# Kernel optimization log

Measured on AMD Instinct MI355X. Metric: run time of the kernel, lower is better.

Reference implementation:

```python
import jax, jax.numpy as jnp
import numpy as np
import math

H = 8
C = 512
HIDE = 2048
LN_EPS = 1e-6


def setup_inputs() -> dict:
    key = jax.random.key(0)
    ks = jax.random.split(key, 9)
    B, N = 4, 2048
    std = 0.02
    return {
        "q": jax.random.normal(ks[0], (B, N, C), jnp.float32),
        "k": jax.random.normal(ks[1], (B, N, C), jnp.float32),
        "v": jax.random.normal(ks[2], (B, N, C), jnp.float32),
        "fc1_w": jax.random.normal(ks[3], (HIDE, C), jnp.float32) * std,
        "fc1_b": jnp.zeros((HIDE,), jnp.float32),
        "fc2_w": jax.random.normal(ks[4], (C, HIDE), jnp.float32) * std,
        "fc2_b": jnp.zeros((C,), jnp.float32),
        "ln1_w": jnp.ones((C,), jnp.float32),
        "ln1_b": jnp.zeros((C,), jnp.float32),
        "ln2_w": jnp.ones((C,), jnp.float32),
        "ln2_b": jnp.zeros((C,), jnp.float32),
    }


def _layernorm(x, w, b):
    mu = jnp.mean(x, axis=-1, keepdims=True)
    var = jnp.var(x, axis=-1, keepdims=True)
    return (x - mu) * jax.lax.rsqrt(var + LN_EPS) * w + b


def _mha(q, k, v):
    B, N, _ = q.shape
    hd = C // H
    # [B, H, N, hd]
    qh = q.reshape(B, N, H, hd).transpose(0, 2, 1, 3)
    kh = k.reshape(B, N, H, hd).transpose(0, 2, 1, 3)
    vh = v.reshape(B, N, H, hd).transpose(0, 2, 1, 3)
    scores = jnp.einsum('bhqd,bhkd->bhqk', qh, kh) / math.sqrt(hd)
    probs = jax.nn.softmax(scores, axis=-1)
    out = jnp.einsum('bhqk,bhkd->bhqd', probs, vh)
    return out.transpose(0, 2, 1, 3).reshape(B, N, C)


def reference(q, k, v, fc1_w, fc1_b, fc2_w, fc2_b, ln1_w, ln1_b, ln2_w, ln2_b):
    attn = _mha(q, k, v)
    q2 = _layernorm(q + attn, ln1_w, ln1_b)
    h = jax.nn.gelu(q2 @ fc1_w.T + fc1_b, approximate=False)
    mlp = h @ fc2_w.T + fc2_b
    return _layernorm(q2 + mlp, ln2_w, ln2_b)
```

## Files before the change

kernel.cpp:

```cpp
#include <hip/hip_runtime.h>
#include <math.h>

typedef unsigned short u16;
typedef __bf16 bf16_t;
typedef bf16_t bf16x4 __attribute__((ext_vector_type(4)));
typedef bf16_t bf16x8 __attribute__((ext_vector_type(8)));
typedef short s16x4 __attribute__((ext_vector_type(4)));
typedef float f32x4 __attribute__((ext_vector_type(4)));

typedef const __attribute__((address_space(1))) void* gcp;
typedef __attribute__((address_space(3))) void* lcp;

#define BB 4
#define NN 2048
#define CC 512
#define HH 8
#define HD 64
#define HIDE_ 2048
#define TT (BB*NN)

#if __has_builtin(__builtin_amdgcn_exp2f)
#define EXP2(x) __builtin_amdgcn_exp2f(x)
#else
#define EXP2(x) __expf((x) * 0.69314718055994531f)
#endif

#if __has_builtin(__builtin_amdgcn_rcpf)
#define RCP(x) __builtin_amdgcn_rcpf(x)
#else
#define RCP(x) (1.0f / (x))
#endif

__device__ __forceinline__ u16 f2bf(float f) {
  unsigned u = __float_as_uint(f);
  u += 0x7FFF + ((u >> 16) & 1);
  return (u16)(u >> 16);
}

__device__ __forceinline__ int xcd_swz(int orig, int nwg) {
  return (orig & 7) * (nwg >> 3) + (orig >> 3);
}

__device__ __forceinline__ void bf8_to_f(const u16* p, float* f) {
  uint4 u = *(const uint4*)p;
  f[0] = __uint_as_float(u.x << 16); f[1] = __uint_as_float(u.x & 0xffff0000u);
  f[2] = __uint_as_float(u.y << 16); f[3] = __uint_as_float(u.y & 0xffff0000u);
  f[4] = __uint_as_float(u.z << 16); f[5] = __uint_as_float(u.z & 0xffff0000u);
  f[6] = __uint_as_float(u.w << 16); f[7] = __uint_as_float(u.w & 0xffff0000u);
}

__device__ __forceinline__ bf16x8 ldq8(const float* p, float s) {
  float4 a = *(const float4*)p;
  float4 b = *(const float4*)(p + 4);
  bf16x8 r = {(bf16_t)(a.x * s), (bf16_t)(a.y * s), (bf16_t)(a.z * s), (bf16_t)(a.w * s),
              (bf16_t)(b.x * s), (bf16_t)(b.y * s), (bf16_t)(b.z * s), (bf16_t)(b.w * s)};
  return r;
}

__device__ __forceinline__ float gelu_tanh(float x) {
  float y = 0.7978845608028654f * x * (1.0f + 0.044715f * x * x);
  float a = y * 2.8853900817779268f;
  a = fminf(fmaxf(a, -30.0f), 30.0f);
  float e = EXP2(a);
  float t = (e - 1.0f) * RCP(e + 1.0f);
  return 0.5f * x * (1.0f + t);
}

__global__ __launch_bounds__(256) void prep_kernel(const float* __restrict__ k,
                                                   const float* __restrict__ fc1w,
                                                   const float* __restrict__ fc2w,
                                                   const float* __restrict__ v,
                                                   u16* __restrict__ kb,
                                                   u16* __restrict__ w1b,
                                                   u16* __restrict__ w2b,
                                                   u16* __restrict__ vtb) {
  __shared__ __align__(16) u16 T[64 * 72];
  int bid = blockIdx.x, tid = threadIdx.x;
  if (bid < 3072) {
    const float* in;
    u16* out;
    int rel;
    if (bid < 2048)      { in = k;    out = kb;  rel = bid; }
    else if (bid < 2560) { in = fc1w; out = w1b; rel = bid - 2048; }
    else                 { in = fc2w; out = w2b; rel = bid - 2560; }
    int i = (rel * 256 + tid) * 8;
    float4 a = *(const float4*)(in + i);
    float4 b2 = *(const float4*)(in + i + 4);
    u16 r[8] = {f2bf(a.x), f2bf(a.y), f2bf(a.z), f2bf(a.w),
                f2bf(b2.x), f2bf(b2.y), f2bf(b2.z), f2bf(b2.w)};
    *(uint4*)(out + i) = *(const uint4*)r;
    return;
  }
  int tv = bid - 3072;
  int j0 = (tv & 31) * 64;
  int bh = tv >> 5;
  int b = bh >> 3, h = bh & 7;
#pragma unroll
  for (int i = 0; i < 4; i++) {
    int idx = i * 256 + tid;
    int j = idx >> 4, dq = idx & 15;
    float4 a = *(const float4*)(v + ((size_t)(b * NN + j0 + j)) * CC + h * 64 + dq * 4);
    T[(dq * 4 + 0) * 72 + j] = f2bf(a.x);
    T[(dq * 4 + 1) * 72 + j] = f2bf(a.y);
    T[(dq * 4 + 2) * 72 + j] = f2bf(a.z);
    T[(dq * 4 + 3) * 72 + j] = f2bf(a.w);
  }
  __syncthreads();
#pragma unroll
  for (int i = 0; i < 2; i++) {
    int idx = i * 256 + tid;
    int d = idx >> 3, jb = idx & 7;
    uint4 val = *(const uint4*)&T[d * 72 + jb * 8];
    *(uint4*)&vtb[((size_t)(bh * 64 + d)) * NN + j0 + jb * 8] = val;
  }
}

__global__ __launch_bounds__(256, 4) void attn_kernel(const float* __restrict__ qf,
                                                      const u16* __restrict__ kb,
                                                      const u16* __restrict__ vtb,
                                                      u16* __restrict__ ou,
                                                      float qs) {
  __shared__ __align__(16) u16 Ks[64 * 64];
  __shared__ __align__(16) u16 Vs[64 * 64];
  int tid = threadIdx.x, wave = tid >> 6, lane = tid & 63;
  int l15 = lane & 15, quad = lane >> 4;
  int r7 = l15 & 7;
  int bid = xcd_swz(blockIdx.x, 512);
  int qt = bid & 15, h = (bid >> 4) & 7, b = bid >> 7;
  int qw = qt * 128 + wave * 32;

  const float* qp = qf + ((size_t)(b * NN + qw + l15)) * CC + h * 64 + quad * 8;
  bf16x8 qfA0 = ldq8(qp, qs);
  bf16x8 qfA1 = ldq8(qp + 32, qs);
  bf16x8 qfB0 = ldq8(qp + (size_t)16 * CC, qs);
  bf16x8 qfB1 = ldq8(qp + (size_t)16 * CC + 32, qs);

  int rl = lane >> 3;
  int cb = (lane & 7) ^ rl;
  int rK = wave * 16 + rl;
  size_t vtbase = ((size_t)(b * HH + h)) * 64 * NN;
  const u16* kp0 = kb + ((size_t)(b * NN + rK)) * CC + h * 64 + cb * 8;
  const u16* kp1 = kp0 + (size_t)8 * CC;
  const u16* vp0 = vtb + vtbase + (size_t)rK * NN + cb * 8;
  const u16* vp1 = vp0 + (size_t)8 * NN;
  lcp lK0 = (lcp)&Ks[wave * 16 * 64];
  lcp lK1 = (lcp)&Ks[wave * 16 * 64 + 8 * 64];
  lcp lV0 = (lcp)&Vs[wave * 16 * 64];
  lcp lV1 = (lcp)&Vs[wave * 16 * 64 + 8 * 64];

  float lA = 0.f, lB = 0.f;
  f32x4 oA[4] = {}, oB[4] = {};

  for (int kt = 0; kt < 32; kt++) {
    __syncthreads();
    __builtin_amdgcn_global_load_lds((gcp)kp0, lK0, 16, 0, 0);
    __builtin_amdgcn_global_load_lds((gcp)kp1, lK1, 16, 0, 0);
    __builtin_amdgcn_global_load_lds((gcp)vp0, lV0, 16, 0, 0);
    __builtin_amdgcn_global_load_lds((gcp)vp1, lV1, 16, 0, 0);
    kp0 += (size_t)64 * CC; kp1 += (size_t)64 * CC;
    vp0 += 64; vp1 += 64;
    __syncthreads();

    s16x4 pfA[4], pfB[4];
    __builtin_amdgcn_s_setprio(1);
#pragma unroll
    for (int nt = 0; nt < 4; nt++) {
      const u16* krow = &Ks[(nt * 16 + l15) * 64];
      bf16x8 k0 = *(const bf16x8*)&krow[(quad ^ r7) * 8];
      bf16x8 k1 = *(const bf16x8*)&krow[((quad + 4) ^ r7) * 8];
      f32x4 zA = {0.f, 0.f, 0.f, 0.f}, zB = {0.f, 0.f, 0.f, 0.f};
      zA = __builtin_amdgcn_mfma_f32_16x16x32_bf16(k0, qfA0, zA, 0, 0, 0);
      zA = __builtin_amdgcn_mfma_f32_16x16x32_bf16(k1, qfA1, zA, 0, 0, 0);
      zB = __builtin_amdgcn_mfma_f32_16x16x32_bf16(k0, qfB0, zB, 0, 0, 0);
      zB = __builtin_amdgcn_mfma_f32_16x16x32_bf16(k1, qfB1, zB, 0, 0, 0);
      float a0 = EXP2(zA[0]), a1 = EXP2(zA[1]), a2 = EXP2(zA[2]), a3 = EXP2(zA[3]);
      float b0 = EXP2(zB[0]), b1 = EXP2(zB[1]), b2 = EXP2(zB[2]), b3 = EXP2(zB[3]);
      lA += (a0 + a1) + (a2 + a3);
      lB += (b0 + b1) + (b2 + b3);
      bf16x4 ta = {(bf16_t)a0, (bf16_t)a1, (bf16_t)a2, (bf16_t)a3};
      bf16x4 tb = {(bf16_t)b0, (bf16_t)b1, (bf16_t)b2, (bf16_t)b3};
      pfA[nt] = __builtin_bit_cast(s16x4, ta);
      pfB[nt] = __builtin_bit_cast(s16x4, tb);
    }
#pragma unroll
    for (int dt = 0; dt < 4; dt++) {
      const u16* vrow = &Vs[(dt * 16 + l15) * 64];
#pragma unroll
      for (int nt = 0; nt < 4; nt++) {
        s16x4 vf = *(const s16x4*)
            &vrow[((nt * 2 + (quad >> 1)) ^ r7) * 8 + (quad & 1) * 4];
        oA[dt] = __builtin_amdgcn_mfma_f32_16x16x16bf16_1k(vf, pfA[nt], oA[dt], 0, 0, 0);
        oB[dt] = __builtin_amdgcn_mfma_f32_16x16x16bf16_1k(vf, pfB[nt], oB[dt], 0, 0, 0);
      }
    }
    __builtin_amdgcn_s_setprio(0);
  }

  lA += __shfl_xor(lA, 16, 64);
  lA += __shfl_xor(lA, 32, 64);
  lB += __shfl_xor(lB, 16, 64);
  lB += __shfl_xor(lB, 32, 64);
  float invA = 1.0f / lA;
  float invB = 1.0f / lB;
  size_t obase = ((size_t)(b * NN + qw + l15)) * CC + h * 64 + quad * 4;
#pragma unroll
  for (int dt = 0; dt < 4; dt++) {
    u16 ra[4] = {f2bf(oA[dt][0] * invA), f2bf(oA[dt][1] * invA),
                 f2bf(oA[dt][2] * invA), f2bf(oA[dt][3] * invA)};
    u16 rb[4] = {f2bf(oB[dt][0] * invB), f2bf(oB[dt][1] * invB),
                 f2bf(oB[dt][2] * invB), f2bf(oB[dt][3] * invB)};
    *(uint2*)&ou[obase + dt * 16] = *(const uint2*)ra;
    *(uint2*)&ou[obase + (size_t)16 * CC + dt * 16] = *(const uint2*)rb;
  }
}

__global__ __launch_bounds__(256) void ln1_kernel(const float* __restrict__ q,
                                                  const u16* __restrict__ ou,
                                                  const float* __restrict__ w,
                                                  const float* __restrict__ bb,
                                                  u16* __restrict__ outb) {
  int tid = threadIdx.x;
  int row = blockIdx.x * 4 + (tid >> 6);
  int lane = tid & 63;
  size_t base = (size_t)row * CC + lane * 8;
  float4 a0 = *(const float4*)(q + base);
  float4 a1 = *(const float4*)(q + base + 4);
  float c[8];
  bf8_to_f(ou + base, c);
  float av[8] = {a0.x, a0.y, a0.z, a0.w, a1.x, a1.y, a1.z, a1.w};
  float x[8];
#pragma unroll
  for (int i = 0; i < 8; i++) x[i] = av[i] + c[i];
  float sum = 0.f, sq = 0.f;
#pragma unroll
  for (int i = 0; i < 8; i++) { sum += x[i]; sq += x[i] * x[i]; }
#pragma unroll
  for (int msk = 1; msk < 64; msk <<= 1) {
    sum += __shfl_xor(sum, msk, 64);
    sq += __shfl_xor(sq, msk, 64);
  }
  float mu = sum * (1.0f / CC);
  float var = sq * (1.0f / CC) - mu * mu;
  float rs = rsqrtf(var + 1e-6f);
  int col = lane * 8;
  float4 w0 = *(const float4*)(w + col);
  float4 w1 = *(const float4*)(w + col + 4);
  float4 b0 = *(const float4*)(bb + col);
  float4 b1 = *(const float4*)(bb + col + 4);
  float wv[8] = {w0.x, w0.y, w0.z, w0.w, w1.x, w1.y, w1.z, w1.w};
  float bv[8] = {b0.x, b0.y, b0.z, b0.w, b1.x, b1.y, b1.z, b1.w};
  u16 r[8];
#pragma unroll
  for (int i = 0; i < 8; i++) r[i] = f2bf((x[i] - mu) * rs * wv[i] + bv[i]);
  *(uint4*)(outb + base) = *(const uint4*)r;
}

__global__ __launch_bounds__(256) void ln2_kernel(const u16* __restrict__ q2b,
                                                  const u16* __restrict__ mp,
                                                  const float* __restrict__ fb,
                                                  const float* __restrict__ w,
                                                  const float* __restrict__ bb,
                                                  float* __restrict__ outf) {
  int tid = threadIdx.x;
  int row = blockIdx.x * 4 + (tid >> 6);
  int lane = tid & 63;
  size_t base = (size_t)row * CC + lane * 8;
  const u16* mp1 = mp + (size_t)TT * CC;
  int col = lane * 8;
  float a[8], c[8], d[8];
  bf8_to_f(q2b + base, a);
  bf8_to_f(mp + base, c);
  bf8_to_f(mp1 + base, d);
  float4 f0 = *(const float4*)(fb + col);
  float4 f1 = *(const float4*)(fb + col + 4);
  float fbv[8] = {f0.x, f0.y, f0.z, f0.w, f1.x, f1.y, f1.z, f1.w};
  float x[8];
#pragma unroll
  for (int i = 0; i < 8; i++) x[i] = a[i] + (c[i] + d[i]) + fbv[i];
  float sum = 0.f, sq = 0.f;
#pragma unroll
  for (int i = 0; i < 8; i++) { sum += x[i]; sq += x[i] * x[i]; }
#pragma unroll
  for (int msk = 1; msk < 64; msk <<= 1) {
    sum += __shfl_xor(sum, msk, 64);
    sq += __shfl_xor(sq, msk, 64);
  }
  float mu = sum * (1.0f / CC);
  float var = sq * (1.0f / CC) - mu * mu;
  float rs = rsqrtf(var + 1e-6f);
  float4 w0 = *(const float4*)(w + col);
  float4 w1 = *(const float4*)(w + col + 4);
  float4 b0 = *(const float4*)(bb + col);
  float4 b1 = *(const float4*)(bb + col + 4);
  float wv[8] = {w0.x, w0.y, w0.z, w0.w, w1.x, w1.y, w1.z, w1.w};
  float bv[8] = {b0.x, b0.y, b0.z, b0.w, b1.x, b1.y, b1.z, b1.w};
  float y[8];
#pragma unroll
  for (int i = 0; i < 8; i++) y[i] = (x[i] - mu) * rs * wv[i] + bv[i];
  *(float4*)(outf + base) = make_float4(y[0], y[1], y[2], y[3]);
  *(float4*)(outf + base + 4) = make_float4(y[4], y[5], y[6], y[7]);
}

template <bool GELU>
__global__ __launch_bounds__(256) void gemm128(const u16* __restrict__ A,
                                               const u16* __restrict__ Bw,
                                               const float* __restrict__ bias,
                                               u16* __restrict__ outb,
                                               int Nn, int K, int NT,
                                               int gx, int gy) {
  __shared__ __align__(16) u16 As[2][128 * 64];
  __shared__ __align__(16) u16 Bs[2][128 * 64];
  int tid = threadIdx.x, wave = tid >> 6, lane = tid & 63;
  int l15 = lane & 15, quad = lane >> 4;
  int r7 = l15 & 7;
  int l = xcd_swz(blockIdx.x, gridDim.x);
  int bx = l % gx;
  int by = (l / gx) % gy;
  int bz = l / (gx * gy);
  int m0 = by * 128, n0 = bx * 128;
  int kbeg = bz * (NT * 64);
  u16* outz = outb + (size_t)bz * ((size_t)TT * CC);
  int wm = (wave >> 1) * 64, wn = (wave & 1) * 64;
  int w32 = wave * 32;
  int rl = lane >> 3;
  int cb = (lane & 7) ^ rl;
  const u16* Ap = &A[(size_t)(m0 + w32 + rl) * K + kbeg + cb * 8];
  const u16* Bp = &Bw[(size_t)(n0 + w32 + rl) * K + kbeg + cb * 8];
  unsigned sb = w32 * 64;

  f32x4 acc[4][4] = {};

  auto stage = [&](int buf, int kofs) {
#pragma unroll
    for (int c = 0; c < 4; c++) {
      __builtin_amdgcn_global_load_lds((gcp)(Ap + kofs + (size_t)(c * 8) * K),
          (lcp)&As[buf][sb + c * 512], 16, 0, 0);
      __builtin_amdgcn_global_load_lds((gcp)(Bp + kofs + (size_t)(c * 8) * K),
          (lcp)&Bs[buf][sb + c * 512], 16, 0, 0);
    }
  };

  stage(0, 0);
  stage(1, 64);
  asm volatile("s_waitcnt vmcnt(8)" ::: "memory");
  __builtin_amdgcn_s_barrier();

  for (int t = 0; t < NT; t++) {
    int buf = t & 1;
    bool pf = (t + 2) < NT;
    bf16x8 aF[4][2], bF[4][2];
#pragma unroll
    for (int m = 0; m < 4; m++)
#pragma unroll
      for (int kh = 0; kh < 2; kh++)
        aF[m][kh] = *(const bf16x8*)&As[buf][(wm + m * 16 + l15) * 64 +
                                            ((kh * 4 + quad) ^ r7) * 8];
#pragma unroll
    for (int n = 0; n < 4; n++)
#pragma unroll
      for (int kh = 0; kh < 2; kh++)
        bF[n][kh] = *(const bf16x8*)&Bs[buf][(wn + n * 16 + l15) * 64 +
                                            ((kh * 4 + quad) ^ r7) * 8];
    __builtin_amdgcn_s_setprio(1);
#pragma unroll
    for (int m = 0; m < 4; m++)
#pragma unroll
      for (int n = 0; n < 2; n++)
#pragma unroll
        for (int kh = 0; kh < 2; kh++)
          acc[m][n] = __builtin_amdgcn_mfma_f32_16x16x32_bf16(aF[m][kh], bF[n][kh],
                                                              acc[m][n], 0, 0, 0);
    __builtin_amdgcn_s_setprio(0);
    asm volatile("s_waitcnt lgkmcnt(0)\n\ts_barrier" ::: "memory");
    if (pf) stage(buf, (t + 2) * 64);
    __builtin_amdgcn_s_setprio(1);
#pragma unroll
    for (int m = 0; m < 4; m++)
#pragma unroll
      for (int n = 2; n < 4; n++)
#pragma unroll
        for (int kh = 0; kh < 2; kh++)
          acc[m][n] = __builtin_amdgcn_mfma_f32_16x16x32_bf16(aF[m][kh], bF[n][kh],
                                                              acc[m][n], 0, 0, 0);
    __builtin_amdgcn_s_setprio(0);
    if (t + 1 < NT) {
      if (pf) asm volatile("s_waitcnt vmcnt(8)" ::: "memory");
      else    asm volatile("s_waitcnt vmcnt(0)" ::: "memory");
      __builtin_amdgcn_s_barrier();
      asm volatile("" ::: "memory");
    }
  }

#pragma unroll
  for (int am = 0; am < 4; am++)
#pragma unroll
    for (int bn = 0; bn < 4; bn++) {
      int rowi = m0 + wm + am * 16 + quad * 4;
      int col = n0 + wn + bn * 16 + l15;
      float bcol = GELU ? bias[col] : 0.0f;
#pragma unroll
      for (int r = 0; r < 4; r++) {
        float val = acc[am][bn][r] + bcol;
        if (GELU) val = gelu_tanh(val);
        outz[(size_t)(rowi + r) * Nn + col] = f2bf(val);
      }
    }
}

extern "C" void kernel_launch(void* const* d_in, const int* in_sizes, int n_in,
                              void* d_out, int out_size, void* d_ws, size_t ws_size,
                              hipStream_t stream) {
  const float* q = (const float*)d_in[0];
  const float* k = (const float*)d_in[1];
  const float* v = (const float*)d_in[2];
  const float* fc1_w = (const float*)d_in[3];
  const float* fc1_b = (const float*)d_in[4];
  const float* fc2_w = (const float*)d_in[5];
  const float* fc2_b = (const float*)d_in[6];
  const float* ln1_w = (const float*)d_in[7];
  const float* ln1_b = (const float*)d_in[8];
  const float* ln2_w = (const float*)d_in[9];
  const float* ln2_b = (const float*)d_in[10];
  float* out = (float*)d_out;

  char* ws = (char*)d_ws;
  size_t off = 0;
  u16* kb = (u16*)(ws + off); off += (size_t)TT * CC * 2;
  u16* vtb = (u16*)(ws + off); off += (size_t)TT * CC * 2;
  u16* w1b = (u16*)(ws + off); off += (size_t)HIDE_ * CC * 2;
  u16* w2b = (u16*)(ws + off); off += (size_t)CC * HIDE_ * 2;
  u16* ou = (u16*)(ws + off); off += (size_t)TT * CC * 2;
  u16* q2b = (u16*)(ws + off); off += (size_t)TT * CC * 2;
  u16* hbuf = (u16*)(ws + off); off += (size_t)TT * HIDE_ * 2;
  u16* mp = (u16*)(ws + off); off += (size_t)2 * TT * CC * 2;

  const float QS = 0.18033688011112042f;
  prep_kernel<<<4096, 256, 0, stream>>>(k, fc1_w, fc2_w, v, kb, w1b, w2b, vtb);
  attn_kernel<<<512, 256, 0, stream>>>(q, kb, vtb, ou, QS);
  ln1_kernel<<<2048, 256, 0, stream>>>(q, ou, ln1_w, ln1_b, q2b);
  gemm128<true><<<1024, 256, 0, stream>>>(q2b, w1b, fc1_b, hbuf, HIDE_, CC, 8, 16, 64);
  gemm128<false><<<512, 256, 0, stream>>>(hbuf, w2b, fc2_b, mp, CC, HIDE_, 16, 4, 64);
  ln2_kernel<<<2048, 256, 0, stream>>>(q2b, mp, fc2_b, ln2_w, ln2_b, out);
}
```

Before: 220.7 us.

## Switch MLP GEMMs to 256x256 tiles with 8 waves and phased loads

Both MLP GEMMs now use a 256x256 output tile per 512-thread block instead of 128x128 per 256 threads. The main loop is unrolled over two K steps, and loads for the next tiles are interleaved with MFMA quarter-blocks separated by barriers. The fc2 split-K goes from 2 to 4 partial buffers, and ln2 sums four partials. The larger tile reuses each LDS load more and cuts global traffic, but the grid drops to 256 blocks, which may under-fill the GPU. It also doubles LDS usage and adds more barriers and a larger partial-sum buffer.

```diff
diff --git a/kernel.cpp b/kernel.cpp
--- a/kernel.cpp
+++ b/kernel.cpp
@@ -266,17 +266,21 @@
   int lane = tid & 63;
   size_t base = (size_t)row * CC + lane * 8;
   const u16* mp1 = mp + (size_t)TT * CC;
+  const u16* mp2 = mp + (size_t)2 * TT * CC;
+  const u16* mp3 = mp + (size_t)3 * TT * CC;
   int col = lane * 8;
-  float a[8], c[8], d[8];
+  float a[8], c[8], d[8], e[8], g[8];
   bf8_to_f(q2b + base, a);
   bf8_to_f(mp + base, c);
   bf8_to_f(mp1 + base, d);
+  bf8_to_f(mp2 + base, e);
+  bf8_to_f(mp3 + base, g);
   float4 f0 = *(const float4*)(fb + col);
   float4 f1 = *(const float4*)(fb + col + 4);
   float fbv[8] = {f0.x, f0.y, f0.z, f0.w, f1.x, f1.y, f1.z, f1.w};
   float x[8];
 #pragma unroll
-  for (int i = 0; i < 8; i++) x[i] = a[i] + (c[i] + d[i]) + fbv[i];
+  for (int i = 0; i < 8; i++) x[i] = a[i] + ((c[i] + d[i]) + (e[i] + g[i])) + fbv[i];
   float sum = 0.f, sq = 0.f;
 #pragma unroll
   for (int i = 0; i < 8; i++) { sum += x[i]; sq += x[i] * x[i]; }
@@ -301,15 +305,18 @@
   *(float4*)(outf + base + 4) = make_float4(y[4], y[5], y[6], y[7]);
 }
 
+#define PH_BAR() do { asm volatile("" ::: "memory"); __builtin_amdgcn_s_barrier(); \
+                      asm volatile("" ::: "memory"); } while (0)
+
 template <bool GELU>
-__global__ __launch_bounds__(256) void gemm128(const u16* __restrict__ A,
+__global__ __launch_bounds__(512) void gemm256(const u16* __restrict__ A,
                                                const u16* __restrict__ Bw,
                                                const float* __restrict__ bias,
                                                u16* __restrict__ outb,
                                                int Nn, int K, int NT,
                                                int gx, int gy) {
-  __shared__ __align__(16) u16 As[2][128 * 64];
-  __shared__ __align__(16) u16 Bs[2][128 * 64];
+  __shared__ __align__(16) u16 As[2][256 * 64];
+  __shared__ __align__(16) u16 Bs[2][256 * 64];
   int tid = threadIdx.x, wave = tid >> 6, lane = tid & 63;
   int l15 = lane & 15, quad = lane >> 4;
   int r7 = l15 & 7;
@@ -317,94 +324,154 @@
   int bx = l % gx;
   int by = (l / gx) % gy;
   int bz = l / (gx * gy);
-  int m0 = by * 128, n0 = bx * 128;
+  int m0 = by * 256, n0 = bx * 256;
   int kbeg = bz * (NT * 64);
   u16* outz = outb + (size_t)bz * ((size_t)TT * CC);
-  int wm = (wave >> 1) * 64, wn = (wave & 1) * 64;
-  int w32 = wave * 32;
+  int wm2 = (wave >> 2) * 64;
+  int wn2 = (wave & 3) * 32;
   int rl = lane >> 3;
-  int cb = (lane & 7) ^ rl;
-  const u16* Ap = &A[(size_t)(m0 + w32 + rl) * K + kbeg + cb * 8];
-  const u16* Bp = &Bw[(size_t)(n0 + w32 + rl) * K + kbeg + cb * 8];
-  unsigned sb = w32 * 64;
-
-  f32x4 acc[4][4] = {};
-
-  auto stage = [&](int buf, int kofs) {
-#pragma unroll
-    for (int c = 0; c < 4; c++) {
-      __builtin_amdgcn_global_load_lds((gcp)(Ap + kofs + (size_t)(c * 8) * K),
-          (lcp)&As[buf][sb + c * 512], 16, 0, 0);
-      __builtin_amdgcn_global_load_lds((gcp)(Bp + kofs + (size_t)(c * 8) * K),
-          (lcp)&Bs[buf][sb + c * 512], 16, 0, 0);
+  int scb = (lane & 7) ^ rl;
+  const u16* Abase = A + (size_t)m0 * K + kbeg;
+  const u16* Bbase = Bw + (size_t)n0 * K + kbeg;
+
+  f32x4 acc[8][4] = {};
+
+  auto stgA = [&](int buf, int hb, int kofs) {
+#pragma unroll
+    for (int p = 0; p < 2; p++) {
+      int rw = hb + p * 64 + wave * 8;
+      __builtin_amdgcn_global_load_lds(
+          (gcp)(Abase + (size_t)(rw + rl) * K + kofs + scb * 8),
+          (lcp)&As[buf][rw * 64], 16, 0, 0);
     }
   };
-
-  stage(0, 0);
-  stage(1, 64);
-  asm volatile("s_waitcnt vmcnt(8)" ::: "memory");
+  auto stgB = [&](int buf, int hb, int kofs) {
+#pragma unroll
+    for (int p = 0; p < 2; p++) {
+      int rw = hb + p * 64 + wave * 8;
+      __builtin_amdgcn_global_load_lds(
+          (gcp)(Bbase + (size_t)(rw + rl) * K + kofs + scb * 8),
+          (lcp)&Bs[buf][rw * 64], 16, 0, 0);
+    }
+  };
+
+#define RDA(BUF, ROW) \
+  (*(const bf16x8*)&As[BUF][(ROW) * 64 + ((kh * 4 + quad) ^ r7) * 8])
+#define RDB(BUF, ROW) \
+  (*(const bf16x8*)&Bs[BUF][(ROW) * 64 + ((kh * 4 + quad) ^ r7) * 8])
+#define MFMA16(MB, NB, AF, BF)                                                \
+    __builtin_amdgcn_s_setprio(1);                                           \
+    _Pragma("unroll") for (int m = 0; m < 4; m++)                            \
+    _Pragma("unroll") for (int n = 0; n < 2; n++)                            \
+    _Pragma("unroll") for (int kh = 0; kh < 2; kh++)                         \
+      acc[(MB) + m][(NB) + n] = __builtin_amdgcn_mfma_f32_16x16x32_bf16(     \
+          AF[m][kh], BF[n][kh], acc[(MB) + m][(NB) + n], 0, 0, 0);           \
+    __builtin_amdgcn_s_setprio(0);
+
+  stgA(0, 0, 0); stgB(0, 0, 0); stgB(0, 128, 0); stgA(0, 128, 0);
+  stgA(1, 0, 64); stgB(1, 0, 64); stgB(1, 128, 64);
+  asm volatile("s_waitcnt vmcnt(6)" ::: "memory");
   __builtin_amdgcn_s_barrier();
-
-  for (int t = 0; t < NT; t++) {
-    int buf = t & 1;
-    bool pf = (t + 2) < NT;
-    bf16x8 aF[4][2], bF[4][2];
+  asm volatile("" ::: "memory");
+
+  int NI = NT >> 1;
+  for (int i = 0; i < NI; i++) {
+    bool pf = (i + 1) < NI;
+    int kpe = (2 * i + 2) * 64, kpo = (2 * i + 3) * 64, kodd = (2 * i + 1) * 64;
+    bf16x8 aF[4][2], bLo[2][2], bHi[2][2];
+
 #pragma unroll
     for (int m = 0; m < 4; m++)
 #pragma unroll
-      for (int kh = 0; kh < 2; kh++)
-        aF[m][kh] = *(const bf16x8*)&As[buf][(wm + m * 16 + l15) * 64 +
-                                            ((kh * 4 + quad) ^ r7) * 8];
-#pragma unroll
-    for (int n = 0; n < 4; n++)
-#pragma unroll
-      for (int kh = 0; kh < 2; kh++)
-        bF[n][kh] = *(const bf16x8*)&Bs[buf][(wn + n * 16 + l15) * 64 +
-                                            ((kh * 4 + quad) ^ r7) * 8];
-    __builtin_amdgcn_s_setprio(1);
+      for (int kh = 0; kh < 2; kh++) aF[m][kh] = RDA(0, wm2 + m * 16 + l15);
+#pragma unroll
+    for (int n = 0; n < 2; n++)
+#pragma unroll
+      for (int kh = 0; kh < 2; kh++) bLo[n][kh] = RDB(0, wn2 + n * 16 + l15);
+    stgA(1, 128, kodd);
+    PH_BAR();
+    MFMA16(0, 0, aF, bLo)
+    PH_BAR();
+#pragma unroll
+    for (int n = 0; n < 2; n++)
+#pragma unroll
+      for (int kh = 0; kh < 2; kh++) bHi[n][kh] = RDB(0, 128 + wn2 + n * 16 + l15);
+    if (pf) stgA(0, 0, kpe);
+    PH_BAR();
+    MFMA16(0, 2, aF, bHi)
+    PH_BAR();
 #pragma unroll
     for (int m = 0; m < 4; m++)
 #pragma unroll
-      for (int n = 0; n < 2; n++)
-#pragma unroll
-        for (int kh = 0; kh < 2; kh++)
-          acc[m][n] = __builtin_amdgcn_mfma_f32_16x16x32_bf16(aF[m][kh], bF[n][kh],
-                                                              acc[m][n], 0, 0, 0);
-    __builtin_amdgcn_s_setprio(0);
-    asm volatile("s_waitcnt lgkmcnt(0)\n\ts_barrier" ::: "memory");
-    if (pf) stage(buf, (t + 2) * 64);
-    __builtin_amdgcn_s_setprio(1);
+      for (int kh = 0; kh < 2; kh++) aF[m][kh] = RDA(0, 128 + wm2 + m * 16 + l15);
+    if (pf) stgB(0, 0, kpe);
+    PH_BAR();
+    MFMA16(4, 2, aF, bHi)
+    PH_BAR();
+    if (pf) stgB(0, 128, kpe);
+    PH_BAR();
+    MFMA16(4, 0, aF, bLo)
+    if (pf) asm volatile("s_waitcnt vmcnt(6)" ::: "memory");
+    else    asm volatile("s_waitcnt vmcnt(0)" ::: "memory");
+    __builtin_amdgcn_s_barrier();
+    asm volatile("" ::: "memory");
+
 #pragma unroll
     for (int m = 0; m < 4; m++)
 #pragma unroll
-      for (int n = 2; n < 4; n++)
-#pragma unroll
-        for (int kh = 0; kh < 2; kh++)
-          acc[m][n] = __builtin_amdgcn_mfma_f32_16x16x32_bf16(aF[m][kh], bF[n][kh],
-                                                              acc[m][n], 0, 0, 0);
-    __builtin_amdgcn_s_setprio(0);
-    if (t + 1 < NT) {
-      if (pf) asm volatile("s_waitcnt vmcnt(8)" ::: "memory");
-      else    asm volatile("s_waitcnt vmcnt(0)" ::: "memory");
+      for (int kh = 0; kh < 2; kh++) aF[m][kh] = RDA(1, wm2 + m * 16 + l15);
+#pragma unroll
+    for (int n = 0; n < 2; n++)
+#pragma unroll
+      for (int kh = 0; kh < 2; kh++) bLo[n][kh] = RDB(1, wn2 + n * 16 + l15);
+    if (pf) stgA(0, 128, kpe);
+    PH_BAR();
+    MFMA16(0, 0, aF, bLo)
+    PH_BAR();
+#pragma unroll
+    for (int n = 0; n < 2; n++)
+#pragma unroll
+      for (int kh = 0; kh < 2; kh++) bHi[n][kh] = RDB(1, 128 + wn2 + n * 16 + l15);
+    if (pf) stgA(1, 0, kpo);
+    PH_BAR();
+    MFMA16(0, 2, aF, bHi)
+    PH_BAR();
+#pragma unroll
+    for (int m = 0; m < 4; m++)
+#pragma unroll
+      for (int kh = 0; kh < 2; kh++) aF[m][kh] = RDA(1, 128 + wm2 + m * 16 + l15);
+    if (pf) stgB(1, 0, kpo);
+    PH_BAR();
+    MFMA16(4, 2, aF, bHi)
+    PH_BAR();
+    if (pf) stgB(1, 128, kpo);
+    PH_BAR();
+    MFMA16(4, 0, aF, bLo)
+    if (pf) {
+      asm volatile("s_waitcnt vmcnt(6)" ::: "memory");
       __builtin_amdgcn_s_barrier();
       asm volatile("" ::: "memory");
     }
   }
-
-#pragma unroll
-  for (int am = 0; am < 4; am++)
-#pragma unroll
-    for (int bn = 0; bn < 4; bn++) {
-      int rowi = m0 + wm + am * 16 + quad * 4;
-      int col = n0 + wn + bn * 16 + l15;
+#undef RDA
+#undef RDB
+#undef MFMA16
+
+#pragma unroll
+  for (int m = 0; m < 8; m++) {
+    int rowi = m0 + ((m >> 2) ? 128 : 0) + wm2 + (m & 3) * 16 + quad * 4;
+#pragma unroll
+    for (int n = 0; n < 4; n++) {
+      int col = n0 + ((n >> 1) ? 128 : 0) + wn2 + (n & 1) * 16 + l15;
       float bcol = GELU ? bias[col] : 0.0f;
 #pragma unroll
       for (int r = 0; r < 4; r++) {
-        float val = acc[am][bn][r] + bcol;
+        float val = acc[m][n][r] + bcol;
         if (GELU) val = gelu_tanh(val);
         outz[(size_t)(rowi + r) * Nn + col] = f2bf(val);
       }
     }
+  }
 }
 
 extern "C" void kernel_launch(void* const* d_in, const int* in_sizes, int n_in,
@@ -432,13 +499,13 @@
   u16* ou = (u16*)(ws + off); off += (size_t)TT * CC * 2;
   u16* q2b = (u16*)(ws + off); off += (size_t)TT * CC * 2;
   u16* hbuf = (u16*)(ws + off); off += (size_t)TT * HIDE_ * 2;
-  u16* mp = (u16*)(ws + off); off += (size_t)2 * TT * CC * 2;
+  u16* mp = (u16*)(ws + off); off += (size_t)4 * TT * CC * 2;
 
   const float QS = 0.18033688011112042f;
   prep_kernel<<<4096, 256, 0, stream>>>(k, fc1_w, fc2_w, v, kb, w1b, w2b, vtb);
   attn_kernel<<<512, 256, 0, stream>>>(q, kb, vtb, ou, QS);
   ln1_kernel<<<2048, 256, 0, stream>>>(q, ou, ln1_w, ln1_b, q2b);
-  gemm128<true><<<1024, 256, 0, stream>>>(q2b, w1b, fc1_b, hbuf, HIDE_, CC, 8, 16, 64);
-  gemm128<false><<<512, 256, 0, stream>>>(hbuf, w2b, fc2_b, mp, CC, HIDE_, 16, 4, 64);
+  gemm256<true><<<256, 512, 0, stream>>>(q2b, w1b, fc1_b, hbuf, HIDE_, CC, 8, 8, 32);
+  gemm256<false><<<256, 512, 0, stream>>>(hbuf, w2b, fc2_b, mp, CC, HIDE_, 8, 2, 32);
   ln2_kernel<<<2048, 256, 0, stream>>>(q2b, mp, fc2_b, ln2_w, ln2_b, out);
 }
```

Measured after the change: 222.7 us. About the same (+0.9%).
